# Kernel optimization log

Measured on AMD Instinct MI355X. Metric: run time of the kernel, lower is better.

## Reference

```python
import jax, jax.numpy as jnp
import numpy as np

B, P = 4, 65536
TD, HID, OUT = 32, 128, 4
RES = 256
NFREQ = 6
CD = 3 * 2 * NFREQ  # frequency encoding out dim


def setup_inputs() -> dict:
    key = jax.random.key(0)
    ks = jax.random.split(key, 12)

    def w(k, shape):
        fan_in = shape[-1]
        return jax.random.normal(k, shape, jnp.float32) / np.sqrt(fan_in)

    return {
        "triplane": jax.random.normal(ks[0], (3 * B, TD, RES, RES), jnp.float32),
        "coords": jax.random.uniform(ks[1], (B, P, 3), jnp.float32),  # inside aabb [-1,1]^3
        "w_in": w(ks[2], (HID, TD + CD)),
        "b_in": jnp.zeros((HID,), jnp.float32),
        "w_skip": w(ks[3], (HID, TD + CD)),
        "b_skip": jnp.zeros((HID,), jnp.float32),
        "w_before": w(ks[4], (2, HID, HID)),
        "b_before": jnp.zeros((2, HID), jnp.float32),
        "w_after": w(ks[5], (2, HID, HID)),
        "b_after": jnp.zeros((2, HID), jnp.float32),
        "w_out": w(ks[6], (OUT, HID)),
        "b_out": jnp.zeros((OUT,), jnp.float32),
    }


@jax.custom_vjp
def trunc_exp(x):
    return jnp.exp(x)


def _trunc_exp_fwd(x):
    return jnp.exp(x), x


def _trunc_exp_bwd(x, g):
    return (g * jnp.exp(jnp.clip(x, -15.0, 15.0)),)


trunc_exp.defvjp(_trunc_exp_fwd, _trunc_exp_bwd)


def grid_sample_bilinear(feat, gx, gy):
    # feat: [N, C, H, W]; gx, gy: [N, Q] in [-1, 1]; align_corners=True, zero padding.
    N, C, H, W = feat.shape
    ix = (gx + 1.0) * 0.5 * (W - 1)
    iy = (gy + 1.0) * 0.5 * (H - 1)
    x0 = jnp.floor(ix)
    y0 = jnp.floor(iy)
    wx1 = ix - x0
    wy1 = iy - y0
    feat_flat = feat.reshape(N, C, H * W)

    def gather(xf, yf):
        xi = xf.astype(jnp.int32)
        yi = yf.astype(jnp.int32)
        valid = ((xi >= 0) & (xi < W) & (yi >= 0) & (yi < H)).astype(feat.dtype)
        xi = jnp.clip(xi, 0, W - 1)
        yi = jnp.clip(yi, 0, H - 1)
        idx = yi * W + xi  # [N, Q]
        g = jnp.take_along_axis(feat_flat, idx[:, None, :], axis=2)  # [N, C, Q]
        return g * valid[:, None, :]

    out = (
        gather(x0, y0) * ((1 - wx1) * (1 - wy1))[:, None, :]
        + gather(x0 + 1, y0) * (wx1 * (1 - wy1))[:, None, :]
        + gather(x0, y0 + 1) * ((1 - wx1) * wy1)[:, None, :]
        + gather(x0 + 1, y0 + 1) * (wx1 * wy1)[:, None, :]
    )
    return out  # [N, C, Q]


def freq_encode(x):
    # x: [B, P, 3] in [0, 1]; NeRF-style frequency encoding (tcnn 'Frequency').
    freqs = (2.0 ** jnp.arange(NFREQ, dtype=x.dtype)) * jnp.pi  # [NFREQ]
    ang = x[..., :, None] * freqs  # [B, P, 3, NFREQ]
    enc = jnp.concatenate([jnp.sin(ang), jnp.cos(ang)], axis=-1)  # [B, P, 3, 2*NFREQ]
    return enc.reshape(x.shape[0], x.shape[1], CD)


def reference(triplane, coords, w_in, b_in, w_skip, b_skip, w_before, b_before,
              w_after, b_after, w_out, b_out):
    aabb_min = jnp.full((3,), -1.0, jnp.float32)
    aabb_max = jnp.full((3,), 1.0, jnp.float32)

    scaled = 2.0 * (coords - aabb_min) / (aabb_max - aabb_min) - 1.0  # [-1,1]
    norm = (coords - aabb_min) / (aabb_max - aabb_min)  # [0,1]
    selector = jnp.all((norm > 0.0) & (norm < 1.0), axis=-1)  # [B, P]

    # planes: xy=(x,y), xz=(x,z), zy=(y,z); stacked per batch -> [3B, P, 2]
    coords_xy = scaled[:, :, (0, 1)]
    coords_xz = scaled[:, :, (0, 2)]
    coords_zy = scaled[:, :, (1, 2)]
    grid = jnp.stack([coords_xy, coords_xz, coords_zy], axis=1).reshape(3 * B, P, 2)

    feats = grid_sample_bilinear(triplane, grid[..., 0], grid[..., 1])  # [3B, TD, P]
    feats = feats.transpose(0, 2, 1).reshape(B, 3, P, TD).sum(axis=1)  # [B, P, TD]

    h = jnp.concatenate([freq_encode(norm), feats], axis=-1)  # [B, P, CD+TD]

    lin = lambda x, w, b: jnp.einsum("bpf,hf->bph", x, w) + b
    x = jax.nn.relu(lin(h, w_in, b_in))
    for i in range(w_before.shape[0]):
        x = jax.nn.relu(lin(x, w_before[i], b_before[i]))
    x = x + jax.nn.relu(lin(h, w_skip, b_skip))
    for i in range(w_after.shape[0]):
        x = jax.nn.relu(lin(x, w_after[i], b_after[i]))
    x = lin(x, w_out, b_out)  # [B, P, 4]

    rgb = jax.nn.sigmoid(x[..., :3])
    density = trunc_exp(x[..., 3:4] - 1.0) * selector[..., None].astype(x.dtype)
    return rgb, density
```

## Files before the change

kernel.cpp:

```cpp
#include <hip/hip_runtime.h>
#include <stdint.h>

typedef short short8 __attribute__((ext_vector_type(8)));
typedef float floatx16 __attribute__((ext_vector_type(16)));
typedef unsigned int uint32;

#define NPTS (4 * 65536)
#define RGB_OFF (NPTS * 3)

__device__ __forceinline__ uint16_t bf_rne(float f) {
  uint32 u = __float_as_uint(f);
  u += 0x7FFFu + ((u >> 16) & 1u);
  return (uint16_t)(u >> 16);
}
__device__ __forceinline__ uint32 pack2(float a, float b) {
  return __builtin_amdgcn_perm(__float_as_uint(b) + 0x8000u,
                               __float_as_uint(a) + 0x8000u, 0x07060302u);
}
__device__ __forceinline__ float bf_lo(uint32 u) { return __uint_as_float(u << 16); }
__device__ __forceinline__ float bf_hi(uint32 u) { return __uint_as_float(u & 0xFFFF0000u); }
__device__ __forceinline__ void swap32(uint32& a, uint32& b) {
  asm("v_permlane32_swap_b32 %0, %1" : "+v"(a), "+v"(b));
}
__device__ __forceinline__ void gacc(const uint16_t* p, float w, float* acc) {
  uint4 q = *(const uint4*)p;
  acc[0] += w * bf_lo(q.x);
  acc[1] += w * bf_hi(q.x);
  acc[2] += w * bf_lo(q.y);
  acc[3] += w * bf_hi(q.y);
  acc[4] += w * bf_lo(q.z);
  acc[5] += w * bf_hi(q.z);
  acc[6] += w * bf_lo(q.w);
  acc[7] += w * bf_hi(q.w);
}

__global__ __launch_bounds__(256) void k_tr(const float* __restrict__ tri,
                                            uint16_t* __restrict__ out) {
  const size_t P = (size_t)blockIdx.x * 256 + threadIdx.x;
  const int n = (int)(P >> 16);
  const int rem = (int)(P & 65535);
  const float* src = tri + ((size_t)n << 21) + rem;
  uint32 q[16];
#pragma unroll
  for (int c = 0; c < 16; ++c) {
    float a = src[(size_t)(2 * c) << 16];
    float b = src[(size_t)(2 * c + 1) << 16];
    q[c] = pack2(a, b);
  }
  uint4* dst = (uint4*)(out + P * 32);
  dst[0] = make_uint4(q[0], q[1], q[2], q[3]);
  dst[1] = make_uint4(q[4], q[5], q[6], q[7]);
  dst[2] = make_uint4(q[8], q[9], q[10], q[11]);
  dst[3] = make_uint4(q[12], q[13], q[14], q[15]);
}

__global__ __launch_bounds__(256) void k_pack(
    const float* __restrict__ w_in, const float* __restrict__ w_skip,
    const float* __restrict__ w_before, const float* __restrict__ w_after,
    const float* __restrict__ w_out, const float* __restrict__ b_in,
    const float* __restrict__ b_skip, const float* __restrict__ b_before,
    const float* __restrict__ b_after, const float* __restrict__ b_out,
    uint16_t* __restrict__ wpack, float* __restrict__ bpack) {
  const int blk = blockIdx.x;
  if (blk >= 44) {
    for (int t = threadIdx.x; t < 800; t += 256) {
      int l, idx;
      if (t < 768) { l = t >> 7; idx = t & 127; }
      else { l = 6; idx = t - 768; }
      int mt = idx >> 5, rem = idx & 31;
      int half = rem >> 4, r = rem & 15;
      int f = mt * 32 + (r & 3) + 8 * (r >> 2) + 4 * half;
      float v;
      switch (l) {
        case 0: v = b_in[f]; break;
        case 1: v = b_before[f]; break;
        case 2: v = b_before[128 + f]; break;
        case 3: v = b_skip[f]; break;
        case 4: v = b_after[f]; break;
        case 5: v = b_after[128 + f]; break;
        default: v = (f < 4) ? b_out[f] : 0.0f; break;
      }
      bpack[l * 128 + idx] = v;
    }
    return;
  }
  const int w = blk * 4 + (threadIdx.x >> 6);
  const int L = threadIdx.x & 63;
  int lay, mt, k;
  if (w < 20)      { lay = 0; mt = w / 5;        k = w - mt * 5; }
  else if (w < 52) { int u = w - 20;  lay = 1; mt = u >> 3; k = u & 7; }
  else if (w < 84) { int u = w - 52;  lay = 2; mt = u >> 3; k = u & 7; }
  else if (w < 104){ int u = w - 84;  lay = 3; mt = u / 5;  k = u - mt * 5; }
  else if (w < 136){ int u = w - 104; lay = 4; mt = u >> 3; k = u & 7; }
  else if (w < 168){ int u = w - 136; lay = 5; mt = u >> 3; k = u & 7; }
  else             { lay = 6; mt = 0; k = w - 168; }
  const float* W;
  int insk = 0;
  switch (lay) {
    case 0: W = w_in; insk = 1; break;
    case 1: W = w_before; break;
    case 2: W = w_before + 16384; break;
    case 3: W = w_skip; insk = 1; break;
    case 4: W = w_after; break;
    case 5: W = w_after + 16384; break;
    default: W = w_out; break;
  }
  const int frow = mt * 32 + (L & 31);
  const int kbase = k * 16 + (L >> 5) * 8;
  uint16_t h[8];
#pragma unroll
  for (int j = 0; j < 8; ++j) {
    int kl = kbase + j;
    float v;
    if (insk) {
      int col = (kl < 32) ? (36 + kl) : ((kl < 68) ? (kl - 32) : -1);
      v = (col < 0) ? 0.0f : W[frow * 68 + col];
    } else if (lay == 6) {
      v = (frow < 4) ? W[frow * 128 + kl] : 0.0f;
    } else {
      v = W[frow * 128 + kl];
    }
    h[j] = bf_rne(v);
  }
  uint4 q;
  q.x = (uint32)h[0] | ((uint32)h[1] << 16);
  q.y = (uint32)h[2] | ((uint32)h[3] << 16);
  q.z = (uint32)h[4] | ((uint32)h[5] << 16);
  q.w = (uint32)h[6] | ((uint32)h[7] << 16);
  *(uint4*)(wpack + (size_t)w * 512 + L * 8) = q;
}

template <int NFRAG>
__device__ __forceinline__ void stage(const uint16_t* __restrict__ wp_base,
                                      uint16_t* __restrict__ wbuf, int t) {
#pragma unroll
  for (int i = 0; i < NFRAG * 64 / 256; ++i) {
    const int g = t + i * 256;
    uint4 v = *(const uint4*)(wp_base + g * 8);
    *(uint4*)(wbuf + g * 8) = v;
  }
}

template <int LAY, int Ks>
__device__ __forceinline__ void mfma_block(floatx16* a, const short8* bin,
                                           const uint16_t* __restrict__ wbuf,
                                           const float* __restrict__ bpack, int L,
                                           int kh) {
#pragma unroll
  for (int mt = 0; mt < 4; ++mt) {
    const float4* bp = (const float4*)(bpack + LAY * 128 + mt * 32 + kh * 16);
#pragma unroll
    for (int g = 0; g < 4; ++g) {
      float4 v = bp[g];
      a[mt][4 * g + 0] = v.x; a[mt][4 * g + 1] = v.y;
      a[mt][4 * g + 2] = v.z; a[mt][4 * g + 3] = v.w;
    }
  }
  const uint16_t* wp = wbuf + L * 8;
#pragma unroll
  for (int k = 0; k < Ks; ++k) {
    short8 w0 = *(const short8*)(wp + (size_t)(0 * Ks + k) * 512);
    short8 w1 = *(const short8*)(wp + (size_t)(1 * Ks + k) * 512);
    short8 w2 = *(const short8*)(wp + (size_t)(2 * Ks + k) * 512);
    short8 w3 = *(const short8*)(wp + (size_t)(3 * Ks + k) * 512);
    a[0] = __builtin_amdgcn_mfma_f32_32x32x16_bf16(w0, bin[k], a[0], 0, 0, 0);
    a[1] = __builtin_amdgcn_mfma_f32_32x32x16_bf16(w1, bin[k], a[1], 0, 0, 0);
    a[2] = __builtin_amdgcn_mfma_f32_32x32x16_bf16(w2, bin[k], a[2], 0, 0, 0);
    a[3] = __builtin_amdgcn_mfma_f32_32x32x16_bf16(w3, bin[k], a[3], 0, 0, 0);
  }
}

template <int LAY, int Ks>
__device__ __forceinline__ void layer_dense(const short8* bin, short8* bout,
                                            const uint16_t* __restrict__ wbuf,
                                            const float* __restrict__ bpack, int L,
                                            int kh) {
  floatx16 a[4];
  mfma_block<LAY, Ks>(a, bin, wbuf, bpack, L, kh);
#pragma unroll
  for (int f = 0; f < 8; ++f) {
    const int mt = f >> 1, s = f & 1;
    uint32 q0a = pack2(fmaxf(a[mt][8 * s + 0], 0.f), fmaxf(a[mt][8 * s + 1], 0.f));
    uint32 q0b = pack2(fmaxf(a[mt][8 * s + 2], 0.f), fmaxf(a[mt][8 * s + 3], 0.f));
    uint32 q1a = pack2(fmaxf(a[mt][8 * s + 4], 0.f), fmaxf(a[mt][8 * s + 5], 0.f));
    uint32 q1b = pack2(fmaxf(a[mt][8 * s + 6], 0.f), fmaxf(a[mt][8 * s + 7], 0.f));
    swap32(q0a, q1a);
    swap32(q0b, q1b);
    bout[f] = __builtin_bit_cast(short8, make_uint4(q0a, q0b, q1a, q1b));
  }
}

template <int LAY, int Ks>
__device__ __forceinline__ void layer_skip(const short8* hin, short8* bio,
                                           const uint16_t* __restrict__ wbuf,
                                           const float* __restrict__ bpack, int L,
                                           int kh) {
  floatx16 a[4];
  mfma_block<LAY, Ks>(a, hin, wbuf, bpack, L, kh);
#pragma unroll
  for (int f = 0; f < 8; ++f) {
    const int mt = f >> 1, s = f & 1;
    uint4 old = __builtin_bit_cast(uint4, bio[f]);
    uint32 uA = old.x, uB = old.y, uC = old.z, uD = old.w;
    swap32(uA, uC);
    swap32(uB, uD);
    float r0 = fmaxf(a[mt][8 * s + 0], 0.f) + bf_lo(uA);
    float r1 = fmaxf(a[mt][8 * s + 1], 0.f) + bf_hi(uA);
    float r2 = fmaxf(a[mt][8 * s + 2], 0.f) + bf_lo(uB);
    float r3 = fmaxf(a[mt][8 * s + 3], 0.f) + bf_hi(uB);
    float r4 = fmaxf(a[mt][8 * s + 4], 0.f) + bf_lo(uC);
    float r5 = fmaxf(a[mt][8 * s + 5], 0.f) + bf_hi(uC);
    float r6 = fmaxf(a[mt][8 * s + 6], 0.f) + bf_lo(uD);
    float r7 = fmaxf(a[mt][8 * s + 7], 0.f) + bf_hi(uD);
    uint32 q0a = pack2(r0, r1), q0b = pack2(r2, r3);
    uint32 q1a = pack2(r4, r5), q1b = pack2(r6, r7);
    swap32(q0a, q1a);
    swap32(q0b, q1b);
    bio[f] = __builtin_bit_cast(short8, make_uint4(q0a, q0b, q1a, q1b));
  }
}

__global__ __launch_bounds__(256, 3) void k_main(
    const uint16_t* __restrict__ trit, const float* __restrict__ trif,
    const float* __restrict__ coords, const uint16_t* __restrict__ wpack,
    const float* __restrict__ bpack, float* __restrict__ dout, int fast) {
  __shared__ __align__(16) uint16_t wbuf[16384];
  const int t = threadIdx.x;
  const int L = t & 63;
  const int kh = L >> 5;
  const int p = (t >> 6) * 32 + (L & 31);
  const int pg = blockIdx.x * 128 + p;

  stage<20>(wpack, wbuf, t);

  float cx = coords[pg * 3 + 0], cy = coords[pg * 3 + 1], cz = coords[pg * 3 + 2];
  float f1x = cx + 1.0f, f1y = cy + 1.0f, f1z = cz + 1.0f;
  float nx = f1x * 0.5f, ny = f1y * 0.5f, nz = f1z * 0.5f;
  float sx = f1x - 1.0f, sy = f1y - 1.0f, sz = f1z - 1.0f;
  bool sel = (nx > 0.f) & (nx < 1.f) & (ny > 0.f) & (ny < 1.f) & (nz > 0.f) & (nz < 1.f);
  const int b = pg >> 16;
  float acc[16];
#pragma unroll
  for (int j = 0; j < 16; ++j) acc[j] = 0.f;
#pragma unroll
  for (int pl = 0; pl < 3; ++pl) {
    float gx = (pl == 2) ? sy : sx;
    float gy = (pl == 0) ? sy : sz;
    float ix = ((gx + 1.0f) * 0.5f) * 255.0f;
    float iy = ((gy + 1.0f) * 0.5f) * 255.0f;
    float x0f = floorf(ix), y0f = floorf(iy);
    float wx = ix - x0f, wy = iy - y0f;
    float vx0 = (x0f >= 0.0f && x0f < 256.0f) ? 1.f : 0.f;
    float vx1 = (x0f >= -1.0f && x0f < 255.0f) ? 1.f : 0.f;
    float vy0 = (y0f >= 0.0f && y0f < 256.0f) ? 1.f : 0.f;
    float vy1 = (y0f >= -1.0f && y0f < 255.0f) ? 1.f : 0.f;
    int x0 = min(max((int)x0f, 0), 255), x1 = min(max((int)x0f + 1, 0), 255);
    int y0 = min(max((int)y0f, 0), 255), y1 = min(max((int)y0f + 1, 0), 255);
    float w00 = (1.f - wx) * (1.f - wy) * vx0 * vy0;
    float w10 = wx * (1.f - wy) * vx1 * vy0;
    float w01 = (1.f - wx) * wy * vx0 * vy1;
    float w11 = wx * wy * vx1 * vy1;
    const int n = 3 * b + pl;
    if (fast) {
      const uint16_t* cb = trit + ((size_t)n << 21) + kh * 8;
      size_t o00 = (size_t)(y0 * 256 + x0) << 5, o10 = (size_t)(y0 * 256 + x1) << 5;
      size_t o01 = (size_t)(y1 * 256 + x0) << 5, o11 = (size_t)(y1 * 256 + x1) << 5;
      gacc(cb + o00, w00, acc); gacc(cb + 16 + o00, w00, acc + 8);
      gacc(cb + o10, w10, acc); gacc(cb + 16 + o10, w10, acc + 8);
      gacc(cb + o01, w01, acc); gacc(cb + 16 + o01, w01, acc + 8);
      gacc(cb + o11, w11, acc); gacc(cb + 16 + o11, w11, acc + 8);
    } else {
      const float* basef = trif + (((size_t)n * 32) << 16);
#pragma unroll
      for (int j = 0; j < 8; ++j) {
        const float* c0p = basef + (((size_t)(kh * 8 + j)) << 16);
        const float* c1p = basef + (((size_t)(16 + kh * 8 + j)) << 16);
        acc[j] += w00 * c0p[y0 * 256 + x0] + w10 * c0p[y0 * 256 + x1] +
                  w01 * c0p[y1 * 256 + x0] + w11 * c0p[y1 * 256 + x1];
        acc[8 + j] += w00 * c1p[y0 * 256 + x0] + w10 * c1p[y0 * 256 + x1] +
                      w01 * c1p[y1 * 256 + x0] + w11 * c1p[y1 * 256 + x1];
      }
    }
  }
  short8 hf[5];
  hf[0] = __builtin_bit_cast(
      short8, make_uint4(pack2(acc[0], acc[1]), pack2(acc[2], acc[3]),
                         pack2(acc[4], acc[5]), pack2(acc[6], acc[7])));
  hf[1] = __builtin_bit_cast(
      short8, make_uint4(pack2(acc[8], acc[9]), pack2(acc[10], acc[11]),
                         pack2(acc[12], acc[13]), pack2(acc[14], acc[15])));
  {
    float sv[3][6], cv[3][6];
#pragma unroll
    for (int d = 0; d < 3; ++d) {
      float nd = (d == 0) ? nx : (d == 1) ? ny : nz;
#pragma unroll
      for (int k = 0; k < 6; ++k) {
        float rev = nd * (0.5f * (float)(1 << k));
        float r = rev - rintf(rev);
        sv[d][k] = __builtin_amdgcn_sinf(r);
        cv[d][k] = __builtin_amdgcn_cosf(r);
      }
    }
    if (kh == 0) {
      hf[2] = __builtin_bit_cast(
          short8, make_uint4(pack2(sv[0][0], sv[0][1]), pack2(sv[0][2], sv[0][3]),
                             pack2(sv[0][4], sv[0][5]), pack2(cv[0][0], cv[0][1])));
      hf[3] = __builtin_bit_cast(
          short8, make_uint4(pack2(sv[1][4], sv[1][5]), pack2(cv[1][0], cv[1][1]),
                             pack2(cv[1][2], cv[1][3]), pack2(cv[1][4], cv[1][5])));
      hf[4] = __builtin_bit_cast(
          short8, make_uint4(pack2(cv[2][2], cv[2][3]), pack2(cv[2][4], cv[2][5]), 0u, 0u));
    } else {
      hf[2] = __builtin_bit_cast(
          short8, make_uint4(pack2(cv[0][2], cv[0][3]), pack2(cv[0][4], cv[0][5]),
                             pack2(sv[1][0], sv[1][1]), pack2(sv[1][2], sv[1][3])));
      hf[3] = __builtin_bit_cast(
          short8, make_uint4(pack2(sv[2][0], sv[2][1]), pack2(sv[2][2], sv[2][3]),
                             pack2(sv[2][4], sv[2][5]), pack2(cv[2][0], cv[2][1])));
      hf[4] = __builtin_bit_cast(short8, make_uint4(0u, 0u, 0u, 0u));
    }
  }

  short8 bf[8];
  __syncthreads();
  layer_dense<0, 5>(hf, bf, wbuf, bpack, L, kh);
  __syncthreads(); stage<32>(wpack + (size_t)20 * 512, wbuf, t); __syncthreads();
  layer_dense<1, 8>(bf, bf, wbuf, bpack, L, kh);
  __syncthreads(); stage<32>(wpack + (size_t)52 * 512, wbuf, t); __syncthreads();
  layer_dense<2, 8>(bf, bf, wbuf, bpack, L, kh);
  __syncthreads(); stage<20>(wpack + (size_t)84 * 512, wbuf, t); __syncthreads();
  layer_skip<3, 5>(hf, bf, wbuf, bpack, L, kh);
  __syncthreads(); stage<32>(wpack + (size_t)104 * 512, wbuf, t); __syncthreads();
  layer_dense<4, 8>(bf, bf, wbuf, bpack, L, kh);
  __syncthreads(); stage<32>(wpack + (size_t)136 * 512, wbuf, t); __syncthreads();
  layer_dense<5, 8>(bf, bf, wbuf, bpack, L, kh);
  __syncthreads(); stage<8>(wpack + (size_t)168 * 512, wbuf, t); __syncthreads();

  {
    floatx16 a;
    const float4* bp = (const float4*)(bpack + 768 + kh * 16);
#pragma unroll
    for (int g = 0; g < 4; ++g) {
      float4 v = bp[g];
      a[4 * g + 0] = v.x; a[4 * g + 1] = v.y; a[4 * g + 2] = v.z; a[4 * g + 3] = v.w;
    }
    const uint16_t* wp = wbuf + L * 8;
#pragma unroll
    for (int k = 0; k < 8; ++k) {
      short8 af = *(const short8*)(wp + (size_t)k * 512);
      a = __builtin_amdgcn_mfma_f32_32x32x16_bf16(af, bf[k], a, 0, 0, 0);
    }
    if (kh == 0) {
      const float l2e = 1.44269504f;
      float r0 = 1.0f / (1.0f + exp2f(-l2e * a[0]));
      float r1 = 1.0f / (1.0f + exp2f(-l2e * a[1]));
      float r2 = 1.0f / (1.0f + exp2f(-l2e * a[2]));
      float dens = exp2f((a[3] - 1.0f) * l2e) * (sel ? 1.0f : 0.0f);
      dout[pg * 3 + 0] = r0;
      dout[pg * 3 + 1] = r1;
      dout[pg * 3 + 2] = r2;
      dout[RGB_OFF + pg] = dens;
    }
  }
}

extern "C" void kernel_launch(void* const* d_in, const int* in_sizes, int n_in,
                              void* d_out, int out_size, void* d_ws, size_t ws_size,
                              hipStream_t stream) {
  const float* tri = (const float*)d_in[0];
  const float* coords = (const float*)d_in[1];
  const float* w_in = (const float*)d_in[2];
  const float* b_in = (const float*)d_in[3];
  const float* w_skip = (const float*)d_in[4];
  const float* b_skip = (const float*)d_in[5];
  const float* w_bef = (const float*)d_in[6];
  const float* b_bef = (const float*)d_in[7];
  const float* w_aft = (const float*)d_in[8];
  const float* b_aft = (const float*)d_in[9];
  const float* w_out = (const float*)d_in[10];
  const float* b_out = (const float*)d_in[11];
  const size_t TRI_B = (size_t)12 * 256 * 256 * 32 * 2;
  const size_t WP_B = (size_t)176 * 1024;
  const size_t BP_B = 3200;
  char* ws = (char*)d_ws;
  const int fast = (ws_size >= TRI_B + WP_B + BP_B) ? 1 : 0;
  uint16_t* trit;
  uint16_t* wpk;
  float* bpk;
  if (fast) {
    trit = (uint16_t*)ws;
    wpk = (uint16_t*)(ws + TRI_B);
    bpk = (float*)(ws + TRI_B + WP_B);
  } else {
    trit = (uint16_t*)ws;
    wpk = (uint16_t*)ws;
    bpk = (float*)(ws + WP_B);
  }
  if (fast) k_tr<<<dim3(3072), dim3(256), 0, stream>>>(tri, trit);
  k_pack<<<dim3(45), dim3(256), 0, stream>>>(w_in, w_skip, w_bef, w_aft, w_out,
                                             b_in, b_skip, b_bef, b_aft, b_out,
                                             wpk, bpk);
  k_main<<<dim3(2048), dim3(256), 0, stream>>>(trit, tri, coords, wpk, bpk,
                                               (float*)d_out, fast);
}
```

Before: 268.6 us.

## Pipeline MLP weight staging through a triple-buffered LDS ring with async loads

Replaces the per-layer synchronous global-to-LDS weight staging, which used two barriers per layer, with a three-slot LDS ring filled by global_load_lds direct-to-LDS copies. Each layer is split into K half-chunks, and the next chunks are prefetched while MFMAs consume the current one. Partial vmcnt waits gate each chunk. Weights are repacked into per-half-chunk order, and biases are cached in LDS. This aims to hide weight-load latency behind compute, at the cost of more LDS use (about 52KB), which may reduce occupancy, and fragile hand-tuned waitcnt accounting.

```diff
diff --git a/kernel.cpp b/kernel.cpp
--- a/kernel.cpp
+++ b/kernel.cpp
@@ -7,6 +7,9 @@
 
 #define NPTS (4 * 65536)
 #define RGB_OFF (NPTS * 3)
+
+typedef __attribute__((address_space(1))) void GV;
+typedef __attribute__((address_space(3))) void LV;
 
 __device__ __forceinline__ uint16_t bf_rne(float f) {
   uint32 u = __float_as_uint(f);
@@ -127,28 +130,50 @@
   q.y = (uint32)h[2] | ((uint32)h[3] << 16);
   q.z = (uint32)h[4] | ((uint32)h[5] << 16);
   q.w = (uint32)h[6] | ((uint32)h[7] << 16);
-  *(uint4*)(wpack + (size_t)w * 512 + L * 8) = q;
-}
-
-template <int NFRAG>
-__device__ __forceinline__ void stage(const uint16_t* __restrict__ wp_base,
-                                      uint16_t* __restrict__ wbuf, int t) {
-#pragma unroll
-  for (int i = 0; i < NFRAG * 64 / 256; ++i) {
-    const int g = t + i * 256;
-    uint4 v = *(const uint4*)(wp_base + g * 8);
-    *(uint4*)(wbuf + g * 8) = v;
-  }
-}
-
-template <int LAY, int Ks>
-__device__ __forceinline__ void mfma_block(floatx16* a, const short8* bin,
-                                           const uint16_t* __restrict__ wbuf,
-                                           const float* __restrict__ bpack, int L,
-                                           int kh) {
+  int LBASE;
+  switch (lay) {
+    case 0: LBASE = 0; break;
+    case 1: LBASE = 10240; break;
+    case 2: LBASE = 26624; break;
+    case 3: LBASE = 43008; break;
+    case 4: LBASE = 53248; break;
+    case 5: LBASE = 69632; break;
+    default: LBASE = 86016; break;
+  }
+  const int kh0 = insk ? 3 : 4;
+  const int ksTot = insk ? 5 : 8;
+  const int hh = (k >= kh0) ? 1 : 0;
+  const int ksh = hh ? (ksTot - kh0) : kh0;
+  const int kk = k - hh * kh0;
+  const int h0frags = (lay == 6) ? 4 : kh0 * 4;
+  const size_t off = (size_t)LBASE + (size_t)(hh ? h0frags * 512 : 0) +
+                     (size_t)(mt * ksh + kk) * 512 + (size_t)L * 8;
+  *(uint4*)(wpack + off) = q;
+}
+
+template <int CH>
+__device__ __forceinline__ void stageA(const uint16_t* __restrict__ gp,
+                                       uint16_t* __restrict__ lp, int t) {
+#pragma unroll
+  for (int i = 0; i < CH; ++i) {
+    const int g = (t + i * 256) * 8;
+    __builtin_amdgcn_global_load_lds((GV*)(gp + g), (LV*)(lp + g), 16, 0, 0);
+  }
+  __builtin_amdgcn_sched_barrier(0);
+}
+
+template <int N>
+__device__ __forceinline__ void bar_keep() {
+  asm volatile("s_waitcnt vmcnt(%0) lgkmcnt(0)" :: "i"(N) : "memory");
+  __builtin_amdgcn_s_barrier();
+  asm volatile("" ::: "memory");
+}
+
+__device__ __forceinline__ void acc_init4(floatx16* a, const float* bl, int LAY,
+                                          int kh) {
 #pragma unroll
   for (int mt = 0; mt < 4; ++mt) {
-    const float4* bp = (const float4*)(bpack + LAY * 128 + mt * 32 + kh * 16);
+    const float4* bp = (const float4*)(bl + LAY * 128 + mt * 32 + kh * 16);
 #pragma unroll
     for (int g = 0; g < 4; ++g) {
       float4 v = bp[g];
@@ -156,13 +181,18 @@
       a[mt][4 * g + 2] = v.z; a[mt][4 * g + 3] = v.w;
     }
   }
-  const uint16_t* wp = wbuf + L * 8;
-#pragma unroll
-  for (int k = 0; k < Ks; ++k) {
-    short8 w0 = *(const short8*)(wp + (size_t)(0 * Ks + k) * 512);
-    short8 w1 = *(const short8*)(wp + (size_t)(1 * Ks + k) * 512);
-    short8 w2 = *(const short8*)(wp + (size_t)(2 * Ks + k) * 512);
-    short8 w3 = *(const short8*)(wp + (size_t)(3 * Ks + k) * 512);
+}
+
+template <int KsH>
+__device__ __forceinline__ void chunk4(floatx16* a, const short8* bin,
+                                       const uint16_t* __restrict__ wb, int L) {
+  const uint16_t* wp = wb + L * 8;
+#pragma unroll
+  for (int k = 0; k < KsH; ++k) {
+    short8 w0 = *(const short8*)(wp + (size_t)(0 * KsH + k) * 512);
+    short8 w1 = *(const short8*)(wp + (size_t)(1 * KsH + k) * 512);
+    short8 w2 = *(const short8*)(wp + (size_t)(2 * KsH + k) * 512);
+    short8 w3 = *(const short8*)(wp + (size_t)(3 * KsH + k) * 512);
     a[0] = __builtin_amdgcn_mfma_f32_32x32x16_bf16(w0, bin[k], a[0], 0, 0, 0);
     a[1] = __builtin_amdgcn_mfma_f32_32x32x16_bf16(w1, bin[k], a[1], 0, 0, 0);
     a[2] = __builtin_amdgcn_mfma_f32_32x32x16_bf16(w2, bin[k], a[2], 0, 0, 0);
@@ -170,13 +200,7 @@
   }
 }
 
-template <int LAY, int Ks>
-__device__ __forceinline__ void layer_dense(const short8* bin, short8* bout,
-                                            const uint16_t* __restrict__ wbuf,
-                                            const float* __restrict__ bpack, int L,
-                                            int kh) {
-  floatx16 a[4];
-  mfma_block<LAY, Ks>(a, bin, wbuf, bpack, L, kh);
+__device__ __forceinline__ void epi_dense(const floatx16* a, short8* bout) {
 #pragma unroll
   for (int f = 0; f < 8; ++f) {
     const int mt = f >> 1, s = f & 1;
@@ -190,13 +214,7 @@
   }
 }
 
-template <int LAY, int Ks>
-__device__ __forceinline__ void layer_skip(const short8* hin, short8* bio,
-                                           const uint16_t* __restrict__ wbuf,
-                                           const float* __restrict__ bpack, int L,
-                                           int kh) {
-  floatx16 a[4];
-  mfma_block<LAY, Ks>(a, hin, wbuf, bpack, L, kh);
+__device__ __forceinline__ void epi_skip(const floatx16* a, short8* bio) {
 #pragma unroll
   for (int f = 0; f < 8; ++f) {
     const int mt = f >> 1, s = f & 1;
@@ -224,14 +242,19 @@
     const uint16_t* __restrict__ trit, const float* __restrict__ trif,
     const float* __restrict__ coords, const uint16_t* __restrict__ wpack,
     const float* __restrict__ bpack, float* __restrict__ dout, int fast) {
-  __shared__ __align__(16) uint16_t wbuf[16384];
+  __shared__ __align__(16) uint16_t ring[3][8192];
+  __shared__ __align__(16) float blds[800];
   const int t = threadIdx.x;
   const int L = t & 63;
   const int kh = L >> 5;
   const int p = (t >> 6) * 32 + (L & 31);
   const int pg = blockIdx.x * 128 + p;
 
-  stage<20>(wpack, wbuf, t);
+  stageA<3>(wpack + 0,     ring[0], t);
+  stageA<2>(wpack + 6144,  ring[1], t);
+  stageA<4>(wpack + 10240, ring[2], t);
+  for (int i = t; i < 400; i += 256)
+    ((float2*)blds)[i] = ((const float2*)bpack)[i];
 
   float cx = coords[pg * 3 + 0], cy = coords[pg * 3 + 1], cz = coords[pg * 3 + 2];
   float f1x = cx + 1.0f, f1y = cy + 1.0f, f1z = cz + 1.0f;
@@ -322,41 +345,83 @@
     }
   }
 
+  __syncthreads();
+  floatx16 a[4];
   short8 bf[8];
-  __syncthreads();
-  layer_dense<0, 5>(hf, bf, wbuf, bpack, L, kh);
-  __syncthreads(); stage<32>(wpack + (size_t)20 * 512, wbuf, t); __syncthreads();
-  layer_dense<1, 8>(bf, bf, wbuf, bpack, L, kh);
-  __syncthreads(); stage<32>(wpack + (size_t)52 * 512, wbuf, t); __syncthreads();
-  layer_dense<2, 8>(bf, bf, wbuf, bpack, L, kh);
-  __syncthreads(); stage<20>(wpack + (size_t)84 * 512, wbuf, t); __syncthreads();
-  layer_skip<3, 5>(hf, bf, wbuf, bpack, L, kh);
-  __syncthreads(); stage<32>(wpack + (size_t)104 * 512, wbuf, t); __syncthreads();
-  layer_dense<4, 8>(bf, bf, wbuf, bpack, L, kh);
-  __syncthreads(); stage<32>(wpack + (size_t)136 * 512, wbuf, t); __syncthreads();
-  layer_dense<5, 8>(bf, bf, wbuf, bpack, L, kh);
-  __syncthreads(); stage<8>(wpack + (size_t)168 * 512, wbuf, t); __syncthreads();
+
+  acc_init4(a, blds, 0, kh);
+  chunk4<3>(a, hf, ring[0], L);
+  bar_keep<0>(); stageA<4>(wpack + 18432, ring[0], t);
+  chunk4<2>(a, hf + 3, ring[1], L);
+  bar_keep<4>(); stageA<4>(wpack + 26624, ring[1], t);
+  epi_dense(a, bf);
+
+  acc_init4(a, blds, 1, kh);
+  chunk4<4>(a, bf, ring[2], L);
+  bar_keep<4>(); stageA<4>(wpack + 34816, ring[2], t);
+  chunk4<4>(a, bf + 4, ring[0], L);
+  bar_keep<4>(); stageA<3>(wpack + 43008, ring[0], t);
+  epi_dense(a, bf);
+
+  acc_init4(a, blds, 2, kh);
+  chunk4<4>(a, bf, ring[1], L);
+  bar_keep<3>(); stageA<2>(wpack + 49152, ring[1], t);
+  chunk4<4>(a, bf + 4, ring[2], L);
+  bar_keep<2>(); stageA<4>(wpack + 53248, ring[2], t);
+  epi_dense(a, bf);
+
+  acc_init4(a, blds, 3, kh);
+  chunk4<3>(a, hf, ring[0], L);
+  bar_keep<4>(); stageA<4>(wpack + 61440, ring[0], t);
+  chunk4<2>(a, hf + 3, ring[1], L);
+  bar_keep<4>(); stageA<4>(wpack + 69632, ring[1], t);
+  epi_skip(a, bf);
+
+  acc_init4(a, blds, 4, kh);
+  chunk4<4>(a, bf, ring[2], L);
+  bar_keep<4>(); stageA<4>(wpack + 77824, ring[2], t);
+  chunk4<4>(a, bf + 4, ring[0], L);
+  bar_keep<4>(); stageA<1>(wpack + 86016, ring[0], t);
+  epi_dense(a, bf);
+
+  acc_init4(a, blds, 5, kh);
+  chunk4<4>(a, bf, ring[1], L);
+  bar_keep<1>(); stageA<1>(wpack + 88064, ring[1], t);
+  chunk4<4>(a, bf + 4, ring[2], L);
+  bar_keep<1>();
+  epi_dense(a, bf);
 
   {
-    floatx16 a;
-    const float4* bp = (const float4*)(bpack + 768 + kh * 16);
+    floatx16 ao;
+    const float4* bp = (const float4*)(blds + 768 + kh * 16);
 #pragma unroll
     for (int g = 0; g < 4; ++g) {
       float4 v = bp[g];
-      a[4 * g + 0] = v.x; a[4 * g + 1] = v.y; a[4 * g + 2] = v.z; a[4 * g + 3] = v.w;
-    }
-    const uint16_t* wp = wbuf + L * 8;
-#pragma unroll
-    for (int k = 0; k < 8; ++k) {
-      short8 af = *(const short8*)(wp + (size_t)k * 512);
-      a = __builtin_amdgcn_mfma_f32_32x32x16_bf16(af, bf[k], a, 0, 0, 0);
+      ao[4 * g + 0] = v.x; ao[4 * g + 1] = v.y; ao[4 * g + 2] = v.z; ao[4 * g + 3] = v.w;
+    }
+    {
+      const uint16_t* wp = ring[0] + L * 8;
+#pragma unroll
+      for (int k = 0; k < 4; ++k) {
+        short8 af = *(const short8*)(wp + (size_t)k * 512);
+        ao = __builtin_amdgcn_mfma_f32_32x32x16_bf16(af, bf[k], ao, 0, 0, 0);
+      }
+    }
+    bar_keep<0>();
+    {
+      const uint16_t* wp = ring[1] + L * 8;
+#pragma unroll
+      for (int k = 0; k < 4; ++k) {
+        short8 af = *(const short8*)(wp + (size_t)k * 512);
+        ao = __builtin_amdgcn_mfma_f32_32x32x16_bf16(af, bf[4 + k], ao, 0, 0, 0);
+      }
     }
     if (kh == 0) {
       const float l2e = 1.44269504f;
-      float r0 = 1.0f / (1.0f + exp2f(-l2e * a[0]));
-      float r1 = 1.0f / (1.0f + exp2f(-l2e * a[1]));
-      float r2 = 1.0f / (1.0f + exp2f(-l2e * a[2]));
-      float dens = exp2f((a[3] - 1.0f) * l2e) * (sel ? 1.0f : 0.0f);
+      float r0 = 1.0f / (1.0f + exp2f(-l2e * ao[0]));
+      float r1 = 1.0f / (1.0f + exp2f(-l2e * ao[1]));
+      float r2 = 1.0f / (1.0f + exp2f(-l2e * ao[2]));
+      float dens = exp2f((ao[3] - 1.0f) * l2e) * (sel ? 1.0f : 0.0f);
       dout[pg * 3 + 0] = r0;
       dout[pg * 3 + 1] = r1;
       dout[pg * 3 + 2] = r2;
```

After: 245.6 us, median of 2. 1.09x faster.

## Split gather/encode and MLP into separate kernels and merge prep launches

Applied to the files above, without the earlier changes.

Merges the triplane transpose and weight packing into one prep launch. It also splits the fused main kernel into a gather+encode kernel, which writes bf16 MLP input fragments to workspace, and an MLP kernel that reads them back. The aim is to let the latency-bound gather phase run at full occupancy without the MLP's shared memory and register limits, and to cut one launch. In exchange it adds a global round-trip of about 40 MB of fragment data plus one extra launch. The split path is used only when the workspace is large enough.

```diff
diff --git a/kernel.cpp b/kernel.cpp
--- a/kernel.cpp
+++ b/kernel.cpp
@@ -7,6 +7,7 @@
 
 #define NPTS (4 * 65536)
 #define RGB_OFF (NPTS * 3)
+#define GTOT (2048 * 256)
 
 __device__ __forceinline__ uint16_t bf_rne(float f) {
   uint32 u = __float_as_uint(f);
@@ -34,34 +35,35 @@
   acc[7] += w * bf_hi(q.w);
 }
 
-__global__ __launch_bounds__(256) void k_tr(const float* __restrict__ tri,
-                                            uint16_t* __restrict__ out) {
-  const size_t P = (size_t)blockIdx.x * 256 + threadIdx.x;
-  const int n = (int)(P >> 16);
-  const int rem = (int)(P & 65535);
-  const float* src = tri + ((size_t)n << 21) + rem;
-  uint32 q[16];
-#pragma unroll
-  for (int c = 0; c < 16; ++c) {
-    float a = src[(size_t)(2 * c) << 16];
-    float b = src[(size_t)(2 * c + 1) << 16];
-    q[c] = pack2(a, b);
-  }
-  uint4* dst = (uint4*)(out + P * 32);
-  dst[0] = make_uint4(q[0], q[1], q[2], q[3]);
-  dst[1] = make_uint4(q[4], q[5], q[6], q[7]);
-  dst[2] = make_uint4(q[8], q[9], q[10], q[11]);
-  dst[3] = make_uint4(q[12], q[13], q[14], q[15]);
-}
-
-__global__ __launch_bounds__(256) void k_pack(
+__global__ __launch_bounds__(256) void k_prep(
+    const float* __restrict__ tri, uint16_t* __restrict__ out, int ntr,
     const float* __restrict__ w_in, const float* __restrict__ w_skip,
     const float* __restrict__ w_before, const float* __restrict__ w_after,
     const float* __restrict__ w_out, const float* __restrict__ b_in,
     const float* __restrict__ b_skip, const float* __restrict__ b_before,
     const float* __restrict__ b_after, const float* __restrict__ b_out,
     uint16_t* __restrict__ wpack, float* __restrict__ bpack) {
-  const int blk = blockIdx.x;
+  const int bx = blockIdx.x;
+  if (bx < ntr) {
+    const size_t P = (size_t)bx * 256 + threadIdx.x;
+    const int n = (int)(P >> 16);
+    const int rem = (int)(P & 65535);
+    const float* src = tri + ((size_t)n << 21) + rem;
+    uint32 q[16];
+#pragma unroll
+    for (int c = 0; c < 16; ++c) {
+      float a = src[(size_t)(2 * c) << 16];
+      float b = src[(size_t)(2 * c + 1) << 16];
+      q[c] = pack2(a, b);
+    }
+    uint4* dst = (uint4*)(out + P * 32);
+    dst[0] = make_uint4(q[0], q[1], q[2], q[3]);
+    dst[1] = make_uint4(q[4], q[5], q[6], q[7]);
+    dst[2] = make_uint4(q[8], q[9], q[10], q[11]);
+    dst[3] = make_uint4(q[12], q[13], q[14], q[15]);
+    return;
+  }
+  const int blk = bx - ntr;
   if (blk >= 44) {
     for (int t = threadIdx.x; t < 800; t += 256) {
       int l, idx;
@@ -130,6 +132,93 @@
   *(uint4*)(wpack + (size_t)w * 512 + L * 8) = q;
 }
 
+__device__ __forceinline__ void gather_encode(const uint16_t* __restrict__ trit,
+                                              const float* __restrict__ coords,
+                                              int pg, int kh, uint4* hq,
+                                              bool* selp) {
+  float cx = coords[pg * 3 + 0], cy = coords[pg * 3 + 1], cz = coords[pg * 3 + 2];
+  float f1x = cx + 1.0f, f1y = cy + 1.0f, f1z = cz + 1.0f;
+  float nx = f1x * 0.5f, ny = f1y * 0.5f, nz = f1z * 0.5f;
+  float sx = f1x - 1.0f, sy = f1y - 1.0f, sz = f1z - 1.0f;
+  *selp = (nx > 0.f) & (nx < 1.f) & (ny > 0.f) & (ny < 1.f) & (nz > 0.f) & (nz < 1.f);
+  const int b = pg >> 16;
+  float acc[16];
+#pragma unroll
+  for (int j = 0; j < 16; ++j) acc[j] = 0.f;
+#pragma unroll
+  for (int pl = 0; pl < 3; ++pl) {
+    float gx = (pl == 2) ? sy : sx;
+    float gy = (pl == 0) ? sy : sz;
+    float ix = ((gx + 1.0f) * 0.5f) * 255.0f;
+    float iy = ((gy + 1.0f) * 0.5f) * 255.0f;
+    float x0f = floorf(ix), y0f = floorf(iy);
+    float wx = ix - x0f, wy = iy - y0f;
+    float vx0 = (x0f >= 0.0f && x0f < 256.0f) ? 1.f : 0.f;
+    float vx1 = (x0f >= -1.0f && x0f < 255.0f) ? 1.f : 0.f;
+    float vy0 = (y0f >= 0.0f && y0f < 256.0f) ? 1.f : 0.f;
+    float vy1 = (y0f >= -1.0f && y0f < 255.0f) ? 1.f : 0.f;
+    int x0 = min(max((int)x0f, 0), 255), x1 = min(max((int)x0f + 1, 0), 255);
+    int y0 = min(max((int)y0f, 0), 255), y1 = min(max((int)y0f + 1, 0), 255);
+    float w00 = (1.f - wx) * (1.f - wy) * vx0 * vy0;
+    float w10 = wx * (1.f - wy) * vx1 * vy0;
+    float w01 = (1.f - wx) * wy * vx0 * vy1;
+    float w11 = wx * wy * vx1 * vy1;
+    const int n = 3 * b + pl;
+    const uint16_t* cb = trit + ((size_t)n << 21) + kh * 8;
+    size_t o00 = (size_t)(y0 * 256 + x0) << 5, o10 = (size_t)(y0 * 256 + x1) << 5;
+    size_t o01 = (size_t)(y1 * 256 + x0) << 5, o11 = (size_t)(y1 * 256 + x1) << 5;
+    gacc(cb + o00, w00, acc); gacc(cb + 16 + o00, w00, acc + 8);
+    gacc(cb + o10, w10, acc); gacc(cb + 16 + o10, w10, acc + 8);
+    gacc(cb + o01, w01, acc); gacc(cb + 16 + o01, w01, acc + 8);
+    gacc(cb + o11, w11, acc); gacc(cb + 16 + o11, w11, acc + 8);
+  }
+  hq[0] = make_uint4(pack2(acc[0], acc[1]), pack2(acc[2], acc[3]),
+                     pack2(acc[4], acc[5]), pack2(acc[6], acc[7]));
+  hq[1] = make_uint4(pack2(acc[8], acc[9]), pack2(acc[10], acc[11]),
+                     pack2(acc[12], acc[13]), pack2(acc[14], acc[15]));
+  float sv[3][6], cv[3][6];
+#pragma unroll
+  for (int d = 0; d < 3; ++d) {
+    float nd = (d == 0) ? nx : (d == 1) ? ny : nz;
+#pragma unroll
+    for (int k = 0; k < 6; ++k) {
+      float rev = nd * (0.5f * (float)(1 << k));
+      float r = rev - rintf(rev);
+      sv[d][k] = __builtin_amdgcn_sinf(r);
+      cv[d][k] = __builtin_amdgcn_cosf(r);
+    }
+  }
+  if (kh == 0) {
+    hq[2] = make_uint4(pack2(sv[0][0], sv[0][1]), pack2(sv[0][2], sv[0][3]),
+                       pack2(sv[0][4], sv[0][5]), pack2(cv[0][0], cv[0][1]));
+    hq[3] = make_uint4(pack2(sv[1][4], sv[1][5]), pack2(cv[1][0], cv[1][1]),
+                       pack2(cv[1][2], cv[1][3]), pack2(cv[1][4], cv[1][5]));
+    hq[4] = make_uint4(pack2(cv[2][2], cv[2][3]), pack2(cv[2][4], cv[2][5]), 0u, 0u);
+  } else {
+    hq[2] = make_uint4(pack2(cv[0][2], cv[0][3]), pack2(cv[0][4], cv[0][5]),
+                       pack2(sv[1][0], sv[1][1]), pack2(sv[1][2], sv[1][3]));
+    hq[3] = make_uint4(pack2(sv[2][0], sv[2][1]), pack2(sv[2][2], sv[2][3]),
+                       pack2(sv[2][4], sv[2][5]), pack2(cv[2][0], cv[2][1]));
+    hq[4] = make_uint4(0u, 0u, 0u, 0u);
+  }
+}
+
+__global__ __launch_bounds__(256) void k_gather(const uint16_t* __restrict__ trit,
+                                                const float* __restrict__ coords,
+                                                uint4* __restrict__ hfb) {
+  const int t = threadIdx.x;
+  const int L = t & 63;
+  const int kh = L >> 5;
+  const int p = (t >> 6) * 32 + (L & 31);
+  const int pg = blockIdx.x * 128 + p;
+  const int gid = blockIdx.x * 256 + t;
+  uint4 hq[5];
+  bool sel;
+  gather_encode(trit, coords, pg, kh, hq, &sel);
+#pragma unroll
+  for (int f = 0; f < 5; ++f) hfb[(size_t)f * GTOT + gid] = hq[f];
+}
+
 template <int NFRAG>
 __device__ __forceinline__ void stage(const uint16_t* __restrict__ wp_base,
                                       uint16_t* __restrict__ wbuf, int t) {
@@ -220,6 +309,78 @@
   }
 }
 
+__device__ __forceinline__ void mlp_body(const short8* hf, bool sel,
+                                         const uint16_t* __restrict__ wpack,
+                                         const float* __restrict__ bpack,
+                                         uint16_t* __restrict__ wbuf,
+                                         float* __restrict__ dout, int t, int L,
+                                         int kh, int pg) {
+  short8 bf[8];
+  __syncthreads();
+  layer_dense<0, 5>(hf, bf, wbuf, bpack, L, kh);
+  __syncthreads(); stage<32>(wpack + (size_t)20 * 512, wbuf, t); __syncthreads();
+  layer_dense<1, 8>(bf, bf, wbuf, bpack, L, kh);
+  __syncthreads(); stage<32>(wpack + (size_t)52 * 512, wbuf, t); __syncthreads();
+  layer_dense<2, 8>(bf, bf, wbuf, bpack, L, kh);
+  __syncthreads(); stage<20>(wpack + (size_t)84 * 512, wbuf, t); __syncthreads();
+  layer_skip<3, 5>(hf, bf, wbuf, bpack, L, kh);
+  __syncthreads(); stage<32>(wpack + (size_t)104 * 512, wbuf, t); __syncthreads();
+  layer_dense<4, 8>(bf, bf, wbuf, bpack, L, kh);
+  __syncthreads(); stage<32>(wpack + (size_t)136 * 512, wbuf, t); __syncthreads();
+  layer_dense<5, 8>(bf, bf, wbuf, bpack, L, kh);
+  __syncthreads(); stage<8>(wpack + (size_t)168 * 512, wbuf, t); __syncthreads();
+
+  floatx16 a;
+  const float4* bp = (const float4*)(bpack + 768 + kh * 16);
+#pragma unroll
+  for (int g = 0; g < 4; ++g) {
+    float4 v = bp[g];
+    a[4 * g + 0] = v.x; a[4 * g + 1] = v.y; a[4 * g + 2] = v.z; a[4 * g + 3] = v.w;
+  }
+  const uint16_t* wp = wbuf + L * 8;
+#pragma unroll
+  for (int k = 0; k < 8; ++k) {
+    short8 af = *(const short8*)(wp + (size_t)k * 512);
+    a = __builtin_amdgcn_mfma_f32_32x32x16_bf16(af, bf[k], a, 0, 0, 0);
+  }
+  if (kh == 0) {
+    const float l2e = 1.44269504f;
+    float r0 = 1.0f / (1.0f + exp2f(-l2e * a[0]));
+    float r1 = 1.0f / (1.0f + exp2f(-l2e * a[1]));
+    float r2 = 1.0f / (1.0f + exp2f(-l2e * a[2]));
+    float dens = exp2f((a[3] - 1.0f) * l2e) * (sel ? 1.0f : 0.0f);
+    dout[pg * 3 + 0] = r0;
+    dout[pg * 3 + 1] = r1;
+    dout[pg * 3 + 2] = r2;
+    dout[RGB_OFF + pg] = dens;
+  }
+}
+
+__global__ __launch_bounds__(256, 3) void k_mlp(
+    const float* __restrict__ coords, const uint16_t* __restrict__ wpack,
+    const float* __restrict__ bpack, const uint4* __restrict__ hfb,
+    float* __restrict__ dout) {
+  __shared__ __align__(16) uint16_t wbuf[16384];
+  const int t = threadIdx.x;
+  const int L = t & 63;
+  const int kh = L >> 5;
+  const int p = (t >> 6) * 32 + (L & 31);
+  const int pg = blockIdx.x * 128 + p;
+  const int gid = blockIdx.x * 256 + t;
+
+  stage<20>(wpack, wbuf, t);
+
+  short8 hf[5];
+#pragma unroll
+  for (int f = 0; f < 5; ++f)
+    hf[f] = __builtin_bit_cast(short8, hfb[(size_t)f * GTOT + gid]);
+  float cx = coords[pg * 3 + 0], cy = coords[pg * 3 + 1], cz = coords[pg * 3 + 2];
+  float nx = (cx + 1.0f) * 0.5f, ny = (cy + 1.0f) * 0.5f, nz = (cz + 1.0f) * 0.5f;
+  bool sel = (nx > 0.f) & (nx < 1.f) & (ny > 0.f) & (ny < 1.f) & (nz > 0.f) & (nz < 1.f);
+
+  mlp_body(hf, sel, wpack, bpack, wbuf, dout, t, L, kh, pg);
+}
+
 __global__ __launch_bounds__(256, 3) void k_main(
     const uint16_t* __restrict__ trit, const float* __restrict__ trif,
     const float* __restrict__ coords, const uint16_t* __restrict__ wpack,
@@ -233,43 +394,42 @@
 
   stage<20>(wpack, wbuf, t);
 
-  float cx = coords[pg * 3 + 0], cy = coords[pg * 3 + 1], cz = coords[pg * 3 + 2];
-  float f1x = cx + 1.0f, f1y = cy + 1.0f, f1z = cz + 1.0f;
-  float nx = f1x * 0.5f, ny = f1y * 0.5f, nz = f1z * 0.5f;
-  float sx = f1x - 1.0f, sy = f1y - 1.0f, sz = f1z - 1.0f;
-  bool sel = (nx > 0.f) & (nx < 1.f) & (ny > 0.f) & (ny < 1.f) & (nz > 0.f) & (nz < 1.f);
-  const int b = pg >> 16;
-  float acc[16];
-#pragma unroll
-  for (int j = 0; j < 16; ++j) acc[j] = 0.f;
-#pragma unroll
-  for (int pl = 0; pl < 3; ++pl) {
-    float gx = (pl == 2) ? sy : sx;
-    float gy = (pl == 0) ? sy : sz;
-    float ix = ((gx + 1.0f) * 0.5f) * 255.0f;
-    float iy = ((gy + 1.0f) * 0.5f) * 255.0f;
-    float x0f = floorf(ix), y0f = floorf(iy);
-    float wx = ix - x0f, wy = iy - y0f;
-    float vx0 = (x0f >= 0.0f && x0f < 256.0f) ? 1.f : 0.f;
-    float vx1 = (x0f >= -1.0f && x0f < 255.0f) ? 1.f : 0.f;
-    float vy0 = (y0f >= 0.0f && y0f < 256.0f) ? 1.f : 0.f;
-    float vy1 = (y0f >= -1.0f && y0f < 255.0f) ? 1.f : 0.f;
-    int x0 = min(max((int)x0f, 0), 255), x1 = min(max((int)x0f + 1, 0), 255);
-    int y0 = min(max((int)y0f, 0), 255), y1 = min(max((int)y0f + 1, 0), 255);
-    float w00 = (1.f - wx) * (1.f - wy) * vx0 * vy0;
-    float w10 = wx * (1.f - wy) * vx1 * vy0;
-    float w01 = (1.f - wx) * wy * vx0 * vy1;
-    float w11 = wx * wy * vx1 * vy1;
-    const int n = 3 * b + pl;
-    if (fast) {
-      const uint16_t* cb = trit + ((size_t)n << 21) + kh * 8;
-      size_t o00 = (size_t)(y0 * 256 + x0) << 5, o10 = (size_t)(y0 * 256 + x1) << 5;
-      size_t o01 = (size_t)(y1 * 256 + x0) << 5, o11 = (size_t)(y1 * 256 + x1) << 5;
-      gacc(cb + o00, w00, acc); gacc(cb + 16 + o00, w00, acc + 8);
-      gacc(cb + o10, w10, acc); gacc(cb + 16 + o10, w10, acc + 8);
-      gacc(cb + o01, w01, acc); gacc(cb + 16 + o01, w01, acc + 8);
-      gacc(cb + o11, w11, acc); gacc(cb + 16 + o11, w11, acc + 8);
-    } else {
+  short8 hf[5];
+  bool sel;
+  if (fast) {
+    uint4 hq[5];
+    gather_encode(trit, coords, pg, kh, hq, &sel);
+#pragma unroll
+    for (int f = 0; f < 5; ++f) hf[f] = __builtin_bit_cast(short8, hq[f]);
+  } else {
+    float cx = coords[pg * 3 + 0], cy = coords[pg * 3 + 1], cz = coords[pg * 3 + 2];
+    float f1x = cx + 1.0f, f1y = cy + 1.0f, f1z = cz + 1.0f;
+    float nx = f1x * 0.5f, ny = f1y * 0.5f, nz = f1z * 0.5f;
+    float sx = f1x - 1.0f, sy = f1y - 1.0f, sz = f1z - 1.0f;
+    sel = (nx > 0.f) & (nx < 1.f) & (ny > 0.f) & (ny < 1.f) & (nz > 0.f) & (nz < 1.f);
+    const int b = pg >> 16;
+    float acc[16];
+#pragma unroll
+    for (int j = 0; j < 16; ++j) acc[j] = 0.f;
+#pragma unroll
+    for (int pl = 0; pl < 3; ++pl) {
+      float gx = (pl == 2) ? sy : sx;
+      float gy = (pl == 0) ? sy : sz;
+      float ix = ((gx + 1.0f) * 0.5f) * 255.0f;
+      float iy = ((gy + 1.0f) * 0.5f) * 255.0f;
+      float x0f = floorf(ix), y0f = floorf(iy);
+      float wx = ix - x0f, wy = iy - y0f;
+      float vx0 = (x0f >= 0.0f && x0f < 256.0f) ? 1.f : 0.f;
+      float vx1 = (x0f >= -1.0f && x0f < 255.0f) ? 1.f : 0.f;
+      float vy0 = (y0f >= 0.0f && y0f < 256.0f) ? 1.f : 0.f;
+      float vy1 = (y0f >= -1.0f && y0f < 255.0f) ? 1.f : 0.f;
+      int x0 = min(max((int)x0f, 0), 255), x1 = min(max((int)x0f + 1, 0), 255);
+      int y0 = min(max((int)y0f, 0), 255), y1 = min(max((int)y0f + 1, 0), 255);
+      float w00 = (1.f - wx) * (1.f - wy) * vx0 * vy0;
+      float w10 = wx * (1.f - wy) * vx1 * vy0;
+      float w01 = (1.f - wx) * wy * vx0 * vy1;
+      float w11 = wx * wy * vx1 * vy1;
+      const int n = 3 * b + pl;
       const float* basef = trif + (((size_t)n * 32) << 16);
 #pragma unroll
       for (int j = 0; j < 8; ++j) {
@@ -281,15 +441,12 @@
                       w01 * c1p[y1 * 256 + x0] + w11 * c1p[y1 * 256 + x1];
       }
     }
-  }
-  short8 hf[5];
-  hf[0] = __builtin_bit_cast(
-      short8, make_uint4(pack2(acc[0], acc[1]), pack2(acc[2], acc[3]),
-                         pack2(acc[4], acc[5]), pack2(acc[6], acc[7])));
-  hf[1] = __builtin_bit_cast(
-      short8, make_uint4(pack2(acc[8], acc[9]), pack2(acc[10], acc[11]),
-                         pack2(acc[12], acc[13]), pack2(acc[14], acc[15])));
-  {
+    hf[0] = __builtin_bit_cast(
+        short8, make_uint4(pack2(acc[0], acc[1]), pack2(acc[2], acc[3]),
+                           pack2(acc[4], acc[5]), pack2(acc[6], acc[7])));
+    hf[1] = __builtin_bit_cast(
+        short8, make_uint4(pack2(acc[8], acc[9]), pack2(acc[10], acc[11]),
+                           pack2(acc[12], acc[13]), pack2(acc[14], acc[15])));
     float sv[3][6], cv[3][6];
 #pragma unroll
     for (int d = 0; d < 3; ++d) {
@@ -321,48 +478,7 @@
       hf[4] = __builtin_bit_cast(short8, make_uint4(0u, 0u, 0u, 0u));
     }
   }
-
-  short8 bf[8];
-  __syncthreads();
-  layer_dense<0, 5>(hf, bf, wbuf, bpack, L, kh);
-  __syncthreads(); stage<32>(wpack + (size_t)20 * 512, wbuf, t); __syncthreads();
-  layer_dense<1, 8>(bf, bf, wbuf, bpack, L, kh);
-  __syncthreads(); stage<32>(wpack + (size_t)52 * 512, wbuf, t); __syncthreads();
-  layer_dense<2, 8>(bf, bf, wbuf, bpack, L, kh);
-  __syncthreads(); stage<20>(wpack + (size_t)84 * 512, wbuf, t); __syncthreads();
-  layer_skip<3, 5>(hf, bf, wbuf, bpack, L, kh);
-  __syncthreads(); stage<32>(wpack + (size_t)104 * 512, wbuf, t); __syncthreads();
-  layer_dense<4, 8>(bf, bf, wbuf, bpack, L, kh);
-  __syncthreads(); stage<32>(wpack + (size_t)136 * 512, wbuf, t); __syncthreads();
-  layer_dense<5, 8>(bf, bf, wbuf, bpack, L, kh);
-  __syncthreads(); stage<8>(wpack + (size_t)168 * 512, wbuf, t); __syncthreads();
-
-  {
-    floatx16 a;
-    const float4* bp = (const float4*)(bpack + 768 + kh * 16);
-#pragma unroll
-    for (int g = 0; g < 4; ++g) {
-      float4 v = bp[g];
-      a[4 * g + 0] = v.x; a[4 * g + 1] = v.y; a[4 * g + 2] = v.z; a[4 * g + 3] = v.w;
-    }
-    const uint16_t* wp = wbuf + L * 8;
-#pragma unroll
-    for (int k = 0; k < 8; ++k) {
-      short8 af = *(const short8*)(wp + (size_t)k * 512);
-      a = __builtin_amdgcn_mfma_f32_32x32x16_bf16(af, bf[k], a, 0, 0, 0);
-    }
-    if (kh == 0) {
-      const float l2e = 1.44269504f;
-      float r0 = 1.0f / (1.0f + exp2f(-l2e * a[0]));
-      float r1 = 1.0f / (1.0f + exp2f(-l2e * a[1]));
-      float r2 = 1.0f / (1.0f + exp2f(-l2e * a[2]));
-      float dens = exp2f((a[3] - 1.0f) * l2e) * (sel ? 1.0f : 0.0f);
-      dout[pg * 3 + 0] = r0;
-      dout[pg * 3 + 1] = r1;
-      dout[pg * 3 + 2] = r2;
-      dout[RGB_OFF + pg] = dens;
-    }
-  }
+  mlp_body(hf, sel, wpack, bpack, wbuf, dout, t, L, kh, pg);
 }
 
 extern "C" void kernel_launch(void* const* d_in, const int* in_sizes, int n_in,
@@ -383,24 +499,34 @@
   const size_t TRI_B = (size_t)12 * 256 * 256 * 32 * 2;
   const size_t WP_B = (size_t)176 * 1024;
   const size_t BP_B = 3200;
+  const size_t HF_B = (size_t)5 * GTOT * 16;
   char* ws = (char*)d_ws;
   const int fast = (ws_size >= TRI_B + WP_B + BP_B) ? 1 : 0;
+  const int fast2 = (ws_size >= TRI_B + WP_B + BP_B + HF_B) ? 1 : 0;
   uint16_t* trit;
   uint16_t* wpk;
   float* bpk;
+  uint4* hfb = nullptr;
   if (fast) {
     trit = (uint16_t*)ws;
     wpk = (uint16_t*)(ws + TRI_B);
     bpk = (float*)(ws + TRI_B + WP_B);
+    hfb = (uint4*)(ws + TRI_B + WP_B + BP_B);
   } else {
     trit = (uint16_t*)ws;
     wpk = (uint16_t*)ws;
     bpk = (float*)(ws + WP_B);
   }
-  if (fast) k_tr<<<dim3(3072), dim3(256), 0, stream>>>(tri, trit);
-  k_pack<<<dim3(45), dim3(256), 0, stream>>>(w_in, w_skip, w_bef, w_aft, w_out,
-                                             b_in, b_skip, b_bef, b_aft, b_out,
-                                             wpk, bpk);
-  k_main<<<dim3(2048), dim3(256), 0, stream>>>(trit, tri, coords, wpk, bpk,
-                                               (float*)d_out, fast);
-}
+  const int ntr = fast ? 3072 : 0;
+  k_prep<<<dim3(ntr + 45), dim3(256), 0, stream>>>(
+      tri, trit, ntr, w_in, w_skip, w_bef, w_aft, w_out, b_in, b_skip, b_bef,
+      b_aft, b_out, wpk, bpk);
+  if (fast2) {
+    k_gather<<<dim3(2048), dim3(256), 0, stream>>>(trit, coords, hfb);
+    k_mlp<<<dim3(2048), dim3(256), 0, stream>>>(coords, wpk, bpk, hfb,
+                                                (float*)d_out);
+  } else {
+    k_main<<<dim3(2048), dim3(256), 0, stream>>>(trit, tri, coords, wpk, bpk,
+                                                 (float*)d_out, fast);
+  }
+}
```

Measured after the change: 288.2 us. 1.07x slower.
